# Performance work log

Measured on AMD Instinct MI355X. Metric: run time of the kernel, lower is better.

## Reference

```python
import jax, jax.numpy as jnp
import numpy as np

N_NODES = 100000
N_EDGES = 1600000
D_IN = 128
D_HID = 128
D_OUT = 128
E_DIM = 16


def setup_inputs() -> dict:
    key = jax.random.key(0)
    ks = jax.random.split(key, 8)
    nh = jax.random.normal(ks[0], (N_NODES, D_IN), dtype=jnp.float32)
    eh = jax.random.normal(ks[1], (N_EDGES, E_DIM), dtype=jnp.float32)
    edge_index = jax.random.randint(ks[2], (2, N_EDGES), 0, N_NODES, dtype=jnp.int64)
    # 2-layer MLP params (Linear -> relu -> Linear), Kaiming-ish init
    W1 = jax.random.normal(ks[3], (D_IN, D_HID), dtype=jnp.float32) / np.sqrt(D_IN)
    b1 = jnp.zeros((D_HID,), dtype=jnp.float32)
    W2 = jax.random.normal(ks[4], (D_HID, D_OUT), dtype=jnp.float32) / np.sqrt(D_HID)
    b2 = jnp.zeros((D_OUT,), dtype=jnp.float32)
    return {"nh": nh, "eh": eh, "edge_index": edge_index,
            "W1": W1, "b1": b1, "W2": W2, "b2": b2}


def reference(nh, eh, edge_index, W1, b1, W2, b2):
    src, dst = edge_index[0], edge_index[1]
    n = nh.shape[0]
    # degree of destination nodes via scatter_add of ones
    deg = jax.ops.segment_sum(jnp.ones(dst.shape[0], dtype=nh.dtype), dst,
                              num_segments=n)
    # deg^{-1/2} with inf -> 0 for isolated nodes
    deg_inv_sqrt = jnp.where(deg > 0, jax.lax.rsqrt(jnp.maximum(deg, 1e-30)),
                             jnp.zeros_like(deg))
    # gather source features, scale by deg_inv_sqrt[src]  -> [E, d]
    n_msg = nh[src] * deg_inv_sqrt[src][:, None]
    # scatter_add messages to destinations  -> [N, d]
    agg = jax.ops.segment_sum(n_msg, dst, num_segments=n)
    agg = agg * deg_inv_sqrt[:, None]
    # 2-layer MLP (nf_lin): Linear -> relu -> Linear
    h = jax.nn.relu(agg @ W1 + b1)
    n_h = h @ W2 + b2
    return (n_h, eh)
```

## Files before the change

### kernel.cpp

```cpp
#include <hip/hip_runtime.h>
#include <hip/hip_bf16.h>

#define NNODES 100000
#define NEDGES 1600000
#define DIM 128
#define EDIM 16

#define NBKT 256
#define BW 391
#define CHUNK 4096
#define EPT 16
#define NCHUNK ((NEDGES + CHUNK - 1) / CHUNK)

#define AGG_BLKS 4096
#define CPY_BLKS 1024

#define O_BH     0u
#define O_BOFS   4096u
#define O_BTAIL  8192u
#define O_W1P    16384u
#define O_W2P    49152u
#define O_RP     81920u
#define O_DINV   491520u
#define O_CSR    921600u
#define O_EBUF   7340032u

typedef __attribute__((ext_vector_type(8))) short bf16x8;
typedef __attribute__((ext_vector_type(4))) float f32x4;

__device__ __forceinline__ unsigned rn_bf16(float x) {
    unsigned u = __float_as_uint(x);
    return (u + 0x7FFFu + ((u >> 16) & 1u)) >> 16;
}

__global__ __launch_bounds__(256) void bhist(const int* __restrict__ dst,
                                             int* __restrict__ bh) {
    __shared__ int s[NBKT];
    s[threadIdx.x] = 0;
    __syncthreads();
    for (int e = blockIdx.x * 256 + threadIdx.x; e < NEDGES; e += gridDim.x * 256)
        atomicAdd(&s[dst[e] / BW], 1);
    __syncthreads();
    atomicAdd(&bh[threadIdx.x], s[threadIdx.x]);
}

__global__ __launch_bounds__(256) void bscan(const int* __restrict__ bh,
                                             int* __restrict__ bofs,
                                             int* __restrict__ btail) {
    __shared__ int s[256];
    const int t = threadIdx.x;
    int v = bh[t];
    s[t] = v;
    __syncthreads();
    for (int off = 1; off < 256; off <<= 1) {
        int x = (t >= off) ? s[t - off] : 0;
        __syncthreads();
        s[t] += x;
        __syncthreads();
    }
    int ex = s[t] - v;
    bofs[t] = ex;
    btail[t] = ex;
    if (t == 255) bofs[256] = s[255];
}

__global__ __launch_bounds__(256) void bscatter(const int* __restrict__ src,
                                                const int* __restrict__ dst,
                                                int* __restrict__ btail,
                                                unsigned* __restrict__ ebuf) {
    __shared__ int lcnt[NBKT], lofs[NBKT], lcur[NBKT], gbase[NBKT];
    __shared__ unsigned obuf[CHUNK];
    __shared__ unsigned char qb[CHUNK];
    const int tid = threadIdx.x;
    const int e0 = blockIdx.x * CHUNK;
    const int n = min(CHUNK, NEDGES - e0);

    lcnt[tid] = 0;
    __syncthreads();

    int myb[EPT];
    unsigned myrec[EPT];
#pragma unroll
    for (int k = 0; k < EPT; ++k) {
        int q = k * 256 + tid;
        if (q < n) {
            int e = e0 + q;
            int d = dst[e];
            int bb = d / BW;
            int dl = d - bb * BW;
            myrec[k] = (unsigned)src[e] | ((unsigned)dl << 17);
            myb[k] = bb;
            atomicAdd(&lcnt[bb], 1);
        } else myb[k] = -1;
    }
    __syncthreads();

    const int c = lcnt[tid];
    lofs[tid] = c;
    __syncthreads();
    for (int off = 1; off < 256; off <<= 1) {
        int x = (tid >= off) ? lofs[tid - off] : 0;
        __syncthreads();
        lofs[tid] += x;
        __syncthreads();
    }
    int ex = lofs[tid] - c;
    lofs[tid] = ex;
    lcur[tid] = ex;
    gbase[tid] = atomicAdd(&btail[tid], c);
    __syncthreads();

#pragma unroll
    for (int k = 0; k < EPT; ++k) {
        if (myb[k] >= 0) {
            int p = atomicAdd(&lcur[myb[k]], 1);
            obuf[p] = myrec[k];
            qb[p] = (unsigned char)myb[k];
        }
    }
    __syncthreads();

    for (int q = tid; q < n; q += 256) {
        int bb = qb[q];
        ebuf[gbase[bb] + (q - lofs[bb])] = obuf[q];
    }
}

__global__ __launch_bounds__(256) void csr_build(const unsigned* __restrict__ ebuf,
                                                 const int* __restrict__ bofs,
                                                 int* __restrict__ rp,
                                                 float* __restrict__ dinv,
                                                 int* __restrict__ csr) {
    __shared__ int fcnt[392];
    __shared__ int fcur[392];
    __shared__ int part[49];
    const int b = blockIdx.x, tid = threadIdx.x;
    const int nodebase = b * BW;
    const int nn = min(BW, NNODES - nodebase);
    const int e0 = bofs[b], e1 = bofs[b + 1];

    for (int i = tid; i < 392; i += 256) fcnt[i] = 0;
    __syncthreads();
    for (int q = e0 + tid; q < e1; q += 256)
        atomicAdd(&fcnt[ebuf[q] >> 17], 1);
    __syncthreads();

    if (tid < 49) {
        int s = 0;
#pragma unroll
        for (int k = 0; k < 8; ++k) {
            int idx = 8 * tid + k;
            if (idx < 392) s += fcnt[idx];
        }
        part[tid] = s;
    }
    __syncthreads();
    if (tid == 0) {
        int s = 0;
        for (int k = 0; k < 49; ++k) { int v = part[k]; part[k] = s; s += v; }
    }
    __syncthreads();
    if (tid < 49) {
        int s = part[tid];
#pragma unroll
        for (int k = 0; k < 8; ++k) {
            int idx = 8 * tid + k;
            if (idx < 392) { int v = fcnt[idx]; fcnt[idx] = s; s += v; }
        }
    }
    __syncthreads();

    for (int i = tid; i < nn; i += 256) {
        int deg = fcnt[i + 1] - fcnt[i];
        rp[nodebase + i] = e0 + fcnt[i];
        dinv[nodebase + i] = (deg > 0) ? rsqrtf((float)deg) : 0.0f;
        fcur[i] = fcnt[i];
    }
    if (b == NBKT - 1 && tid == 0) rp[NNODES] = NEDGES;
    __syncthreads();

    for (int q = e0 + tid; q < e1; q += 256) {
        unsigned rec = ebuf[q];
        int dl = rec >> 17;
        int pos = atomicAdd(&fcur[dl], 1);
        csr[e0 + pos] = (int)(rec & 0x1FFFFu);
    }
}

__global__ __launch_bounds__(256) void wpack_kernel(const float* __restrict__ W1,
                                                    const float* __restrict__ W2,
                                                    ushort* __restrict__ w1p,
                                                    ushort* __restrict__ w2p) {
    int idx = blockIdx.x * 256 + threadIdx.x;
    int i = idx & 7;
    int l = (idx >> 3) & 63;
    int c = (idx >> 9) & 7;
    int t = (idx >> 12) & 3;
    int k = 32 * t + 8 * (l >> 4) + i;
    int j = 16 * c + (l & 15);
    w1p[idx] = (ushort)rn_bf16(W1[k * DIM + j]);
    w2p[idx] = (ushort)rn_bf16(W2[k * DIM + j]);
}

__global__ __launch_bounds__(256) void agg_kernel(const int* __restrict__ rp,
                                                  const int* __restrict__ csr,
                                                  const float* __restrict__ dinv,
                                                  const float* __restrict__ nh,
                                                  float* __restrict__ agg,
                                                  const float* __restrict__ eh,
                                                  float* __restrict__ out_eh) {
    if (blockIdx.x >= AGG_BLKS) {
        const float4* s = (const float4*)eh;
        float4* d = (float4*)out_eh;
        const int total = NEDGES * EDIM / 4;
        for (int q = (blockIdx.x - AGG_BLKS) * 256 + threadIdx.x; q < total;
             q += CPY_BLKS * 256)
            d[q] = s[q];
        return;
    }

    const int lane = threadIdx.x & 63;
    const int half = lane >> 5;
    const int l32  = lane & 31;
    const int wid     = (blockIdx.x * 256 + threadIdx.x) >> 6;
    const int nwaves  = (AGG_BLKS * 256) >> 6;

    for (int n = wid; n < NNODES; n += nwaves) {
        const int beg = rp[n];
        const int end = rp[n + 1];
        const float dn = dinv[n];
        float ax = 0.0f, ay = 0.0f, az = 0.0f, aw = 0.0f;

        if (beg < end) {
            const int last = end - 1;
            int c0 = csr[min(beg + 0 + half, last)];
            int c1 = csr[min(beg + 2 + half, last)];
            int c2 = csr[min(beg + 4 + half, last)];
            int c3 = csr[min(beg + 6 + half, last)];
            for (int i = beg; i < end; i += 8) {
                const int inext = i + 8;
                int p0 = c0, p1 = c1, p2 = c2, p3 = c3;
                if (inext < end) {
                    p0 = csr[min(inext + 0 + half, last)];
                    p1 = csr[min(inext + 2 + half, last)];
                    p2 = csr[min(inext + 4 + half, last)];
                    p3 = csr[min(inext + 6 + half, last)];
                }
                float w0 = (i + 0 + half < end) ? dinv[c0] : 0.0f;
                float w1 = (i + 2 + half < end) ? dinv[c1] : 0.0f;
                float w2 = (i + 4 + half < end) ? dinv[c2] : 0.0f;
                float w3 = (i + 6 + half < end) ? dinv[c3] : 0.0f;
                float4 f0 = ((const float4*)(nh + (size_t)c0 * DIM))[l32];
                float4 f1 = ((const float4*)(nh + (size_t)c1 * DIM))[l32];
                float4 f2 = ((const float4*)(nh + (size_t)c2 * DIM))[l32];
                float4 f3 = ((const float4*)(nh + (size_t)c3 * DIM))[l32];
                ax = fmaf(f0.x, w0, ax); ay = fmaf(f0.y, w0, ay);
                az = fmaf(f0.z, w0, az); aw = fmaf(f0.w, w0, aw);
                ax = fmaf(f1.x, w1, ax); ay = fmaf(f1.y, w1, ay);
                az = fmaf(f1.z, w1, az); aw = fmaf(f1.w, w1, aw);
                ax = fmaf(f2.x, w2, ax); ay = fmaf(f2.y, w2, ay);
                az = fmaf(f2.z, w2, az); aw = fmaf(f2.w, w2, aw);
                ax = fmaf(f3.x, w3, ax); ay = fmaf(f3.y, w3, ay);
                az = fmaf(f3.z, w3, az); aw = fmaf(f3.w, w3, aw);
                c0 = p0; c1 = p1; c2 = p2; c3 = p3;
            }
        }

        ax += __shfl_xor(ax, 32);
        ay += __shfl_xor(ay, 32);
        az += __shfl_xor(az, 32);
        aw += __shfl_xor(aw, 32);
        if (half == 0) {
            ((float4*)(agg + (size_t)n * DIM))[l32] =
                make_float4(ax * dn, ay * dn, az * dn, aw * dn);
        }
    }
}

__global__ __launch_bounds__(512) void mlp_mfma(const float* __restrict__ x,
                                                const ushort* __restrict__ w1p,
                                                const ushort* __restrict__ w2p,
                                                const float* __restrict__ b1,
                                                const float* __restrict__ b2,
                                                float* __restrict__ out) {
    __shared__ __align__(16) ushort sW[2][16384];
    __shared__ __align__(16) float  sH[8][2048];

    const int tid  = threadIdx.x;
    const int lane = tid & 63;
    const int w    = tid >> 6;
    const int m    = lane & 15;
    const int g    = lane >> 4;

    {
        const float4* s1 = (const float4*)w1p;
        const float4* s2 = (const float4*)w2p;
        float4* d1 = (float4*)sW[0];
        float4* d2 = (float4*)sW[1];
        for (int q = tid; q < 2048; q += 512) d1[q] = s1[q];
        for (int q = tid; q < 2048; q += 512) d2[q] = s2[q];
    }

    float bias1[8], bias2[8];
#pragma unroll
    for (int c = 0; c < 8; ++c) { bias1[c] = b1[16 * c + m]; bias2[c] = b2[16 * c + m]; }

    __syncthreads();

    const int rowbase = blockIdx.x * 128 + w * 16;
    char* hbase = (char*)sH[w];
    const int node = rowbase + m;
    const bool valid = (node < NNODES);

    f32x4 acc[8];
#pragma unroll
    for (int c = 0; c < 8; ++c) acc[c] = f32x4{0.f, 0.f, 0.f, 0.f};

#pragma unroll
    for (int t = 0; t < 4; ++t) {
        const int kb = 32 * t + 8 * g;
        float4 xa = make_float4(0.f, 0.f, 0.f, 0.f);
        float4 xb = make_float4(0.f, 0.f, 0.f, 0.f);
        if (valid) {
            const float4* px = (const float4*)(x + (size_t)node * DIM + kb);
            xa = px[0];
            xb = px[1];
        }
        float v[8] = {xa.x, xa.y, xa.z, xa.w, xb.x, xb.y, xb.z, xb.w};
        bf16x8 ahi, alo;
#pragma unroll
        for (int i = 0; i < 8; ++i) {
            unsigned hu = rn_bf16(v[i]);
            float hf = __uint_as_float(hu << 16);
            ahi[i] = (short)hu;
            alo[i] = (short)rn_bf16(v[i] - hf);
        }
#pragma unroll
        for (int c = 0; c < 8; ++c) {
            bf16x8 bw = *(const bf16x8*)&sW[0][((t * 8 + c) * 64 + lane) * 8];
            acc[c] = __builtin_amdgcn_mfma_f32_16x16x32_bf16(alo, bw, acc[c], 0, 0, 0);
            acc[c] = __builtin_amdgcn_mfma_f32_16x16x32_bf16(ahi, bw, acc[c], 0, 0, 0);
        }
    }

#pragma unroll
    for (int c = 0; c < 8; ++c) {
#pragma unroll
        for (int r = 0; r < 4; ++r) {
            int row = 4 * g + r;
            float hv = fmaxf(acc[c][r] + bias1[c], 0.0f);
            int off = (row * 512 + (16 * c + m) * 4) ^ ((row & 7) << 4);
            *(float*)(hbase + off) = hv;
        }
    }

#pragma unroll
    for (int c = 0; c < 8; ++c) acc[c] = f32x4{0.f, 0.f, 0.f, 0.f};

#pragma unroll
    for (int t = 0; t < 4; ++t) {
        const int kb = 32 * t + 8 * g;
        int o0 = (m * 512 + kb * 4) ^ ((m & 7) << 4);
        int o1 = (m * 512 + kb * 4 + 16) ^ ((m & 7) << 4);
        f32x4 va = *(const f32x4*)(hbase + o0);
        f32x4 vb = *(const f32x4*)(hbase + o1);
        float v[8] = {va[0], va[1], va[2], va[3], vb[0], vb[1], vb[2], vb[3]};
        bf16x8 ahi, alo;
#pragma unroll
        for (int i = 0; i < 8; ++i) {
            unsigned hu = rn_bf16(v[i]);
            float hf = __uint_as_float(hu << 16);
            ahi[i] = (short)hu;
            alo[i] = (short)rn_bf16(v[i] - hf);
        }
#pragma unroll
        for (int c = 0; c < 8; ++c) {
            bf16x8 bw = *(const bf16x8*)&sW[1][((t * 8 + c) * 64 + lane) * 8];
            acc[c] = __builtin_amdgcn_mfma_f32_16x16x32_bf16(alo, bw, acc[c], 0, 0, 0);
            acc[c] = __builtin_amdgcn_mfma_f32_16x16x32_bf16(ahi, bw, acc[c], 0, 0, 0);
        }
    }

#pragma unroll
    for (int c = 0; c < 8; ++c) {
#pragma unroll
        for (int r = 0; r < 4; ++r) {
            int row = 4 * g + r;
            int off = (row * 512 + (16 * c + m) * 4) ^ ((row & 7) << 4);
            *(float*)(hbase + off) = acc[c][r] + bias2[c];
        }
    }

#pragma unroll
    for (int it = 0; it < 8; ++it) {
        int row = 2 * it + (lane >> 5);
        int c4  = lane & 31;
        int off = (row * 512 + c4 * 16) ^ ((row & 7) << 4);
        f32x4 val = *(const f32x4*)(hbase + off);
        int nodeS = rowbase + row;
        if (nodeS < NNODES)
            *(f32x4*)(out + (size_t)nodeS * DIM + (size_t)c4 * 4) = val;
    }
}

extern "C" void kernel_launch(void* const* d_in, const int* in_sizes, int n_in,
                              void* d_out, int out_size, void* d_ws, size_t ws_size,
                              hipStream_t stream) {
    const float* nh = (const float*)d_in[0];
    const float* eh = (const float*)d_in[1];
    const int*   ei = (const int*)d_in[2];
    const float* W1 = (const float*)d_in[3];
    const float* b1 = (const float*)d_in[4];
    const float* W2 = (const float*)d_in[5];
    const float* b2 = (const float*)d_in[6];

    char* ws = (char*)d_ws;
    int*      bh    = (int*)(ws + O_BH);
    int*      bofs  = (int*)(ws + O_BOFS);
    int*      btail = (int*)(ws + O_BTAIL);
    ushort*   w1p   = (ushort*)(ws + O_W1P);
    ushort*   w2p   = (ushort*)(ws + O_W2P);
    int*      rp    = (int*)(ws + O_RP);
    float*    dinv  = (float*)(ws + O_DINV);
    int*      csr   = (int*)(ws + O_CSR);
    unsigned* ebuf  = (unsigned*)(ws + O_EBUF);

    float* out_nh = (float*)d_out;
    float* out_eh = out_nh + (size_t)NNODES * DIM;

    const int* src = ei;
    const int* dst = ei + NEDGES;

    hipMemsetAsync(bh, 0, NBKT * sizeof(int), stream);

    bhist<<<256, 256, 0, stream>>>(dst, bh);
    bscan<<<1, 256, 0, stream>>>(bh, bofs, btail);
    wpack_kernel<<<64, 256, 0, stream>>>(W1, W2, w1p, w2p);
    bscatter<<<NCHUNK, 256, 0, stream>>>(src, dst, btail, ebuf);
    csr_build<<<NBKT, 256, 0, stream>>>(ebuf, bofs, rp, dinv, csr);
    agg_kernel<<<AGG_BLKS + CPY_BLKS, 256, 0, stream>>>(rp, csr, dinv, nh, out_nh,
                                                        eh, out_eh);
    mlp_mfma<<<(NNODES + 127) / 128, 512, 0, stream>>>(out_nh, w1p, w2p, b1, b2, out_nh);
}
```

Baseline: 468.8 us.

## Gather fp16 copy of node features in aggregation, converting during histogram

Node features are converted once to fp16 in extra blocks fused into the histogram launch, and the aggregation kernel gathers half-precision rows. Each wave now processes four edges per step with 16 lanes per row, and reduces across quarter-waves with shuffles. This halves the bytes of the random gather, which is the dominant memory traffic. The cost is an extra full read and write of the feature matrix and reduced input precision, which may affect accuracy. The CSR prefetch pipelining from the previous version is also dropped.

```diff
diff --git a/kernel.cpp b/kernel.cpp
--- a/kernel.cpp
+++ b/kernel.cpp
@@ -1,5 +1,6 @@
 #include <hip/hip_runtime.h>
 #include <hip/hip_bf16.h>
+#include <hip/hip_fp16.h>
 
 #define NNODES 100000
 #define NEDGES 1600000
@@ -14,6 +15,8 @@
 
 #define AGG_BLKS 4096
 #define CPY_BLKS 1024
+#define HIST_BLKS 256
+#define CVT_BLKS 3072
 
 #define O_BH     0u
 #define O_BOFS   4096u
@@ -24,6 +27,7 @@
 #define O_DINV   491520u
 #define O_CSR    921600u
 #define O_EBUF   7340032u
+#define O_NHH    13740032u
 
 typedef __attribute__((ext_vector_type(8))) short bf16x8;
 typedef __attribute__((ext_vector_type(4))) float f32x4;
@@ -34,11 +38,33 @@
 }
 
 __global__ __launch_bounds__(256) void bhist(const int* __restrict__ dst,
-                                             int* __restrict__ bh) {
+                                             int* __restrict__ bh,
+                                             const float* __restrict__ nh,
+                                             __half* __restrict__ nhh) {
+    if (blockIdx.x >= HIST_BLKS) {
+        const float4* s4 = (const float4*)nh;
+        uint4* d4 = (uint4*)nhh;
+        const int total = NNODES * DIM / 8;
+        for (int q = (blockIdx.x - HIST_BLKS) * 256 + threadIdx.x; q < total;
+             q += CVT_BLKS * 256) {
+            float4 fa = s4[2 * q], fb = s4[2 * q + 1];
+            __half2 h0 = __floats2half2_rn(fa.x, fa.y);
+            __half2 h1 = __floats2half2_rn(fa.z, fa.w);
+            __half2 h2 = __floats2half2_rn(fb.x, fb.y);
+            __half2 h3 = __floats2half2_rn(fb.z, fb.w);
+            uint4 o;
+            o.x = *(const unsigned*)&h0;
+            o.y = *(const unsigned*)&h1;
+            o.z = *(const unsigned*)&h2;
+            o.w = *(const unsigned*)&h3;
+            d4[q] = o;
+        }
+        return;
+    }
     __shared__ int s[NBKT];
     s[threadIdx.x] = 0;
     __syncthreads();
-    for (int e = blockIdx.x * 256 + threadIdx.x; e < NEDGES; e += gridDim.x * 256)
+    for (int e = blockIdx.x * 256 + threadIdx.x; e < NEDGES; e += HIST_BLKS * 256)
         atomicAdd(&s[dst[e] / BW], 1);
     __syncthreads();
     atomicAdd(&bh[threadIdx.x], s[threadIdx.x]);
@@ -205,7 +231,7 @@
 __global__ __launch_bounds__(256) void agg_kernel(const int* __restrict__ rp,
                                                   const int* __restrict__ csr,
                                                   const float* __restrict__ dinv,
-                                                  const float* __restrict__ nh,
+                                                  const __half* __restrict__ nhh,
                                                   float* __restrict__ agg,
                                                   const float* __restrict__ eh,
                                                   float* __restrict__ out_eh) {
@@ -220,8 +246,8 @@
     }
 
     const int lane = threadIdx.x & 63;
-    const int half = lane >> 5;
-    const int l32  = lane & 31;
+    const int q    = lane >> 4;
+    const int l16  = lane & 15;
     const int wid     = (blockIdx.x * 256 + threadIdx.x) >> 6;
     const int nwaves  = (AGG_BLKS * 256) >> 6;
 
@@ -229,50 +255,52 @@
         const int beg = rp[n];
         const int end = rp[n + 1];
         const float dn = dinv[n];
-        float ax = 0.0f, ay = 0.0f, az = 0.0f, aw = 0.0f;
+        float a0 = 0.f, a1 = 0.f, a2 = 0.f, a3 = 0.f;
+        float a4 = 0.f, a5 = 0.f, a6 = 0.f, a7 = 0.f;
 
         if (beg < end) {
             const int last = end - 1;
-            int c0 = csr[min(beg + 0 + half, last)];
-            int c1 = csr[min(beg + 2 + half, last)];
-            int c2 = csr[min(beg + 4 + half, last)];
-            int c3 = csr[min(beg + 6 + half, last)];
             for (int i = beg; i < end; i += 8) {
-                const int inext = i + 8;
-                int p0 = c0, p1 = c1, p2 = c2, p3 = c3;
-                if (inext < end) {
-                    p0 = csr[min(inext + 0 + half, last)];
-                    p1 = csr[min(inext + 2 + half, last)];
-                    p2 = csr[min(inext + 4 + half, last)];
-                    p3 = csr[min(inext + 6 + half, last)];
-                }
-                float w0 = (i + 0 + half < end) ? dinv[c0] : 0.0f;
-                float w1 = (i + 2 + half < end) ? dinv[c1] : 0.0f;
-                float w2 = (i + 4 + half < end) ? dinv[c2] : 0.0f;
-                float w3 = (i + 6 + half < end) ? dinv[c3] : 0.0f;
-                float4 f0 = ((const float4*)(nh + (size_t)c0 * DIM))[l32];
-                float4 f1 = ((const float4*)(nh + (size_t)c1 * DIM))[l32];
-                float4 f2 = ((const float4*)(nh + (size_t)c2 * DIM))[l32];
-                float4 f3 = ((const float4*)(nh + (size_t)c3 * DIM))[l32];
-                ax = fmaf(f0.x, w0, ax); ay = fmaf(f0.y, w0, ay);
-                az = fmaf(f0.z, w0, az); aw = fmaf(f0.w, w0, aw);
-                ax = fmaf(f1.x, w1, ax); ay = fmaf(f1.y, w1, ay);
-                az = fmaf(f1.z, w1, az); aw = fmaf(f1.w, w1, aw);
-                ax = fmaf(f2.x, w2, ax); ay = fmaf(f2.y, w2, ay);
-                az = fmaf(f2.z, w2, az); aw = fmaf(f2.w, w2, aw);
-                ax = fmaf(f3.x, w3, ax); ay = fmaf(f3.y, w3, ay);
-                az = fmaf(f3.z, w3, az); aw = fmaf(f3.w, w3, aw);
-                c0 = p0; c1 = p1; c2 = p2; c3 = p3;
+                const int eA = i + q, eB = i + 4 + q;
+                int ca = csr[min(eA, last)];
+                int cb = csr[min(eB, last)];
+                float wa = (eA < end) ? dinv[ca] : 0.0f;
+                float wb = (eB < end) ? dinv[cb] : 0.0f;
+                uint4 ra = ((const uint4*)(nhh + (size_t)ca * DIM))[l16];
+                uint4 rb = ((const uint4*)(nhh + (size_t)cb * DIM))[l16];
+                float2 f;
+                f = __half22float2(*(const __half2*)&ra.x);
+                a0 = fmaf(f.x, wa, a0); a1 = fmaf(f.y, wa, a1);
+                f = __half22float2(*(const __half2*)&ra.y);
+                a2 = fmaf(f.x, wa, a2); a3 = fmaf(f.y, wa, a3);
+                f = __half22float2(*(const __half2*)&ra.z);
+                a4 = fmaf(f.x, wa, a4); a5 = fmaf(f.y, wa, a5);
+                f = __half22float2(*(const __half2*)&ra.w);
+                a6 = fmaf(f.x, wa, a6); a7 = fmaf(f.y, wa, a7);
+                f = __half22float2(*(const __half2*)&rb.x);
+                a0 = fmaf(f.x, wb, a0); a1 = fmaf(f.y, wb, a1);
+                f = __half22float2(*(const __half2*)&rb.y);
+                a2 = fmaf(f.x, wb, a2); a3 = fmaf(f.y, wb, a3);
+                f = __half22float2(*(const __half2*)&rb.z);
+                a4 = fmaf(f.x, wb, a4); a5 = fmaf(f.y, wb, a5);
+                f = __half22float2(*(const __half2*)&rb.w);
+                a6 = fmaf(f.x, wb, a6); a7 = fmaf(f.y, wb, a7);
             }
         }
 
-        ax += __shfl_xor(ax, 32);
-        ay += __shfl_xor(ay, 32);
-        az += __shfl_xor(az, 32);
-        aw += __shfl_xor(aw, 32);
-        if (half == 0) {
-            ((float4*)(agg + (size_t)n * DIM))[l32] =
-                make_float4(ax * dn, ay * dn, az * dn, aw * dn);
+        a0 += __shfl_xor(a0, 16); a0 += __shfl_xor(a0, 32);
+        a1 += __shfl_xor(a1, 16); a1 += __shfl_xor(a1, 32);
+        a2 += __shfl_xor(a2, 16); a2 += __shfl_xor(a2, 32);
+        a3 += __shfl_xor(a3, 16); a3 += __shfl_xor(a3, 32);
+        a4 += __shfl_xor(a4, 16); a4 += __shfl_xor(a4, 32);
+        a5 += __shfl_xor(a5, 16); a5 += __shfl_xor(a5, 32);
+        a6 += __shfl_xor(a6, 16); a6 += __shfl_xor(a6, 32);
+        a7 += __shfl_xor(a7, 16); a7 += __shfl_xor(a7, 32);
+
+        if (lane < 16) {
+            float4* dst = (float4*)(agg + (size_t)n * DIM + (size_t)l16 * 8);
+            dst[0] = make_float4(a0 * dn, a1 * dn, a2 * dn, a3 * dn);
+            dst[1] = make_float4(a4 * dn, a5 * dn, a6 * dn, a7 * dn);
         }
     }
 }
@@ -424,6 +452,7 @@
     float*    dinv  = (float*)(ws + O_DINV);
     int*      csr   = (int*)(ws + O_CSR);
     unsigned* ebuf  = (unsigned*)(ws + O_EBUF);
+    __half*   nhh   = (__half*)(ws + O_NHH);
 
     float* out_nh = (float*)d_out;
     float* out_eh = out_nh + (size_t)NNODES * DIM;
@@ -433,12 +462,12 @@
 
     hipMemsetAsync(bh, 0, NBKT * sizeof(int), stream);
 
-    bhist<<<256, 256, 0, stream>>>(dst, bh);
+    bhist<<<HIST_BLKS + CVT_BLKS, 256, 0, stream>>>(dst, bh, nh, nhh);
     bscan<<<1, 256, 0, stream>>>(bh, bofs, btail);
     wpack_kernel<<<64, 256, 0, stream>>>(W1, W2, w1p, w2p);
     bscatter<<<NCHUNK, 256, 0, stream>>>(src, dst, btail, ebuf);
     csr_build<<<NBKT, 256, 0, stream>>>(ebuf, bofs, rp, dinv, csr);
-    agg_kernel<<<AGG_BLKS + CPY_BLKS, 256, 0, stream>>>(rp, csr, dinv, nh, out_nh,
+    agg_kernel<<<AGG_BLKS + CPY_BLKS, 256, 0, stream>>>(rp, csr, dinv, nhh, out_nh,
                                                         eh, out_eh);
     mlp_mfma<<<(NNODES + 127) / 128, 512, 0, stream>>>(out_nh, w1p, w2p, b1, b2, out_nh);
 }
```

Result: faster. 426.8 us (-9.0%).
